# Performance work log

Measured on AMD Instinct MI355X. Metric: run time of the kernel, lower is better.

Reference implementation:

```python
import jax, jax.numpy as jnp
import numpy as np

B, DIM, H, W = 8, 128, 64, 64
K = 7                      # involution kernel size
PAD = (K - 1) // 2
GC = 16                    # group_channels (RedNet involution default)
G = DIM // GC              # groups = 8
RED = 4                    # reduction_ratio
BN_EPS = 1e-5
LN_EPS = 1e-6


def setup_inputs() -> dict:
    key = jax.random.key(0)
    ks = jax.random.split(key, 8)
    s = lambda k, sh: jax.random.normal(k, sh, jnp.float32) * 0.02
    return {
        "x": jax.random.normal(ks[0], (B, DIM, H, W), jnp.float32),
        # involution kernel-generation branch: 1x1 conv -> BN -> ReLU -> 1x1 conv
        "conv1_w": s(ks[1], (DIM // RED, DIM)), "conv1_b": jnp.zeros((DIM // RED,), jnp.float32),
        "bn_g": jnp.ones((DIM // RED,), jnp.float32), "bn_b": jnp.zeros((DIM // RED,), jnp.float32),
        "bn_mean": jnp.zeros((DIM // RED,), jnp.float32), "bn_var": jnp.ones((DIM // RED,), jnp.float32),
        "conv2_w": s(ks[2], (K * K * G, DIM // RED)), "conv2_b": jnp.zeros((K * K * G,), jnp.float32),
        # LayerNorm (channels_last)
        "ln_g": jnp.ones((DIM,), jnp.float32), "ln_b": jnp.zeros((DIM,), jnp.float32),
        # pointwise MLP
        "pw1_w": s(ks[3], (2 * DIM, DIM)), "pw1_b": jnp.zeros((2 * DIM,), jnp.float32),
        "pw2_w": s(ks[4], (DIM, 2 * DIM)), "pw2_b": jnp.zeros((DIM,), jnp.float32),
    }


def _involution(x, conv1_w, conv1_b, bn_g, bn_b, bn_mean, bn_var, conv2_w, conv2_b):
    # kernel-generation: 1x1 conv -> BN(eval) -> ReLU -> 1x1 conv
    t = jnp.einsum('oc,bchw->bohw', conv1_w, x) + conv1_b[None, :, None, None]
    scale = bn_g * jax.lax.rsqrt(bn_var + BN_EPS)
    t = t * scale[None, :, None, None] + (bn_b - bn_mean * scale)[None, :, None, None]
    t = jax.nn.relu(t)
    wgt = jnp.einsum('oc,bchw->bohw', conv2_w, t) + conv2_b[None, :, None, None]
    wgt = wgt.reshape(B, G, K * K, H, W)            # per-pixel kernels
    # apply per-pixel kernel: accumulate over window offsets (no unfold materialization)
    xp = jnp.pad(x, ((0, 0), (0, 0), (PAD, PAD), (PAD, PAD)))
    xg = xp.reshape(B, G, GC, H + 2 * PAD, W + 2 * PAD)
    out = jnp.zeros((B, G, GC, H, W), x.dtype)
    for i in range(K):
        for j in range(K):
            patch = xg[:, :, :, i:i + H, j:j + W]   # [B,G,GC,H,W]
            out = out + wgt[:, :, i * K + j][:, :, None] * patch
    return out.reshape(B, DIM, H, W)


def reference(x, conv1_w, conv1_b, bn_g, bn_b, bn_mean, bn_var, conv2_w, conv2_b,
              ln_g, ln_b, pw1_w, pw1_b, pw2_w, pw2_b):
    identity = x
    y = _involution(x, conv1_w, conv1_b, bn_g, bn_b, bn_mean, bn_var, conv2_w, conv2_b)
    y = y.transpose(0, 2, 3, 1)                     # NCHW -> NHWC
    mu = jnp.mean(y, axis=-1, keepdims=True)
    var = jnp.var(y, axis=-1, keepdims=True)
    y = (y - mu) * jax.lax.rsqrt(var + LN_EPS) * ln_g + ln_b
    y = jnp.einsum('bhwc,fc->bhwf', y, pw1_w) + pw1_b
    y = jax.nn.gelu(y, approximate=False)           # torch nn.GELU default (erf)
    # dropout: inference mode -> identity
    y = jnp.einsum('bhwf,cf->bhwc', y, pw2_w) + pw2_b
    y = y.transpose(0, 3, 1, 2)                     # NHWC -> NCHW
    return y + identity
```

## Files before the change

### kernel.cpp

```cpp
#include <hip/hip_runtime.h>
#include <hip/hip_bf16.h>
#include <math.h>

#define Bn   8
#define DIM  128
#define Hs   64
#define Ws   64
#define PADn 3
#define GC   16
#define Gn   8
#define CMID 32
#define NW   392
#define NWP  416

typedef __bf16 bf16x8 __attribute__((ext_vector_type(8)));
typedef float  f32x4  __attribute__((ext_vector_type(4)));
typedef _Float16 h2v  __attribute__((ext_vector_type(2)));
typedef __fp16   fp16x2 __attribute__((ext_vector_type(2)));

__device__ __forceinline__ f32x4 mfma16(bf16x8 a, bf16x8 b, f32x4 c) {
    return __builtin_amdgcn_mfma_f32_16x16x32_bf16(a, b, c, 0, 0, 0);
}

__device__ __forceinline__ __bf16 tobf(float v) {
    __hip_bfloat16 h = __float2bfloat16(v);
    return *reinterpret_cast<__bf16*>(&h);
}

__device__ __forceinline__ unsigned su16(float f) {
    __hip_bfloat16 h = __float2bfloat16(f);
    return (unsigned)*reinterpret_cast<unsigned short*>(&h);
}

__device__ __forceinline__ unsigned pk2u(float a, float b) {
    fp16x2 p = __builtin_amdgcn_cvt_pkrtz(a, b);
    return __builtin_bit_cast(unsigned, p);
}

__device__ __forceinline__ float gelu_t(float v) {
    float u = 0.7978845608f * v * fmaf(0.044715f, v * v, 1.0f);
    float t = __builtin_amdgcn_exp2f(fminf(u, 30.f) * 2.885390082f);
    return v * t * __builtin_amdgcn_rcpf(t + 1.0f);
}

__global__ __launch_bounds__(256) void k0_cvt(const float* __restrict__ w1,
        const float* __restrict__ w2,
        const float* __restrict__ pw1, const float* __restrict__ pw2,
        const float* __restrict__ x,
        __hip_bfloat16* __restrict__ w1b, __hip_bfloat16* __restrict__ w2b,
        __hip_bfloat16* __restrict__ mw1b, __hip_bfloat16* __restrict__ mw2b,
        unsigned* __restrict__ xpair) {
    int T = blockIdx.x * 256 + threadIdx.x;
    if (T < 32768) {
        int i = T;
        if (i < CMID * DIM) w1b[i] = __float2bfloat16(w1[i]);
        if (i < NWP * CMID)
            w2b[i] = (i < NW * CMID) ? __float2bfloat16(w2[i]) : __float2bfloat16(0.f);
        {
            int f = i >> 7, j = i & 127;
            int t4 = j >> 5, k = j & 31;
            int g = k >> 2, pi = (k >> 1) & 1, sel = k & 1;
            mw1b[i] = __float2bfloat16(pw1[f * 128 + g * 16 + t4 * 2 + pi + 8 * sel]);
        }
        mw2b[i] = __float2bfloat16(pw2[i]);
    }
    int c8 = T >> 10;
    int p4 = (T & 1023) * 4;
    int bb = c8 >> 6, gg = (c8 >> 3) & 7, cc = c8 & 7;
    size_t src = ((size_t)(bb * DIM + gg * GC + cc)) * 4096 + p4;
    float4 lo = *(const float4*)&x[src];
    float4 hi = *(const float4*)&x[src + 8 * 4096];
    uint4 o;
    o.x = pk2u(lo.x, hi.x);
    o.y = pk2u(lo.y, hi.y);
    o.z = pk2u(lo.z, hi.z);
    o.w = pk2u(lo.w, hi.w);
    *(uint4*)&xpair[(size_t)c8 * 4096 + p4] = o;
}

__global__ __launch_bounds__(64) void k_all(const float* __restrict__ x,
        const unsigned* __restrict__ xpair,
        const __hip_bfloat16* __restrict__ w1b, const float* __restrict__ b1v,
        const float* __restrict__ bng, const float* __restrict__ bnb,
        const float* __restrict__ bnm, const float* __restrict__ bnv,
        const __hip_bfloat16* __restrict__ w2b, const float* __restrict__ b2v,
        const float* __restrict__ lng, const float* __restrict__ lnb,
        const __hip_bfloat16* __restrict__ mw1b, const float* __restrict__ mb1,
        const __hip_bfloat16* __restrict__ mw2b, const float* __restrict__ mb2,
        float* __restrict__ out) {
    __shared__ __align__(16) char uni[15368];
    h2v* xp    = (h2v*)uni;
    h2v* wgt2  = (h2v*)(uni + 10752);
    __hip_bfloat16* tsh = (__hip_bfloat16*)(uni + 14280);
    __hip_bfloat16* ylds = (__hip_bfloat16*)uni;
    __hip_bfloat16* zsh  = (__hip_bfloat16*)(uni + 4352);

    int bid = blockIdx.x;
    int b = bid & 7;
    int rest = bid >> 3;
    int h = rest >> 2, wq = rest & 3;
    int w0 = wq * 16;
    int lane = threadIdx.x;
    int l15 = lane & 15, l4 = lane >> 4;
    int px = l15, t4 = l4;

    int goff[20];
    unsigned short ldso[20];
#pragma unroll
    for (int e = 0; e < 20; ++e) {
        int i = lane + e * 64;
        int ccp = i / 154;
        int rem = i - ccp * 154;
        int r = rem / 22, col = rem - r * 22;
        int hh = h + r - PADn, wc = w0 + col - PADn;
        bool ok = (i < 1232) & ((unsigned)hh < (unsigned)Hs) & ((unsigned)wc < (unsigned)Ws);
        goff[e] = ok ? (ccp * 4096 + hh * 64 + wc) : -1;
        ldso[e] = (unsigned short)(ccp * 168 + r * 24 + col);
    }

    auto stage = [&](int g, int buf) {
        const unsigned* xg = xpair + (size_t)(b * 64 + g * 8) * 4096;
        unsigned v[20];
#pragma unroll
        for (int e = 0; e < 20; ++e)
            v[e] = (goff[e] >= 0) ? xg[goff[e]] : 0u;
#pragma unroll
        for (int e = 0; e < 20; ++e)
            if (e < 19 || lane < 16)
                *(unsigned*)&xp[buf * 1344 + ldso[e]] = v[e];
    };

    bf16x8 afr[4];
#pragma unroll
    for (int ks = 0; ks < 4; ++ks)
#pragma unroll
        for (int i = 0; i < 8; ++i) {
            int c = ks * 32 + l4 * 8 + i;
            afr[ks][i] = tobf(x[(((size_t)b * DIM + c) * Hs + h) * Ws + w0 + l15]);
        }

    stage(0, 0);

    f32x4 acc1[2];
    acc1[0] = (f32x4){0.f, 0.f, 0.f, 0.f};
    acc1[1] = (f32x4){0.f, 0.f, 0.f, 0.f};
#pragma unroll
    for (int nt = 0; nt < 2; ++nt)
#pragma unroll
        for (int ks = 0; ks < 4; ++ks) {
            bf16x8 bf = *(const bf16x8*)&w1b[(nt * 16 + l15) * DIM + ks * 32 + l4 * 8];
            acc1[nt] = mfma16(afr[ks], bf, acc1[nt]);
        }
#pragma unroll
    for (int nt = 0; nt < 2; ++nt) {
        int o = nt * 16 + l15;
        float sc = bng[o] * rsqrtf(bnv[o] + 1e-5f);
        float sh = bnb[o] - bnm[o] * sc;
        float bv = b1v[o];
#pragma unroll
        for (int r = 0; r < 4; ++r) {
            float v = (acc1[nt][r] + bv) * sc + sh;
            tsh[(l4 * 4 + r) * 34 + o] = __float2bfloat16(fmaxf(v, 0.f));
        }
    }
    bf16x8 a_t = *(const bf16x8*)&tsh[l15 * 34 + l4 * 8];

    unsigned ypk[16];
    float s = 0.f, ss = 0.f;

#pragma unroll 1
    for (int g = 0; g < Gn; ++g) {
        int buf = g & 1;
        if (g == 0) ;
        else stage(g, buf);

        {
            f32x4 ac[4];
#pragma unroll
            for (int nt = 0; nt < 4; ++nt) ac[nt] = (f32x4){0.f, 0.f, 0.f, 0.f};
#pragma unroll
            for (int nt = 0; nt < 4; ++nt) {
                bf16x8 bf = *(const bf16x8*)&w2b[(size_t)(g * 49 + nt * 16 + l15) * CMID + l4 * 8];
                ac[nt] = mfma16(a_t, bf, ac[nt]);
            }
#pragma unroll
            for (int nt = 0; nt < 4; ++nt) {
                int p = nt * 16 + l15;
                if (p < 49) {
                    float bias = b2v[g * 49 + p];
#pragma unroll
                    for (int r = 0; r < 4; ++r) {
                        _Float16 hf16 = (_Float16)(ac[nt][r] + bias);
                        wgt2[p * 18 + l4 * 4 + r] = (h2v){hf16, hf16};
                    }
                }
            }
        }

        h2v wv[49];
#pragma unroll
        for (int p = 0; p < 49; ++p) wv[p] = wgt2[p * 18 + px];

#pragma unroll
        for (int pi = 0; pi < 2; ++pi) {
            int ccp = t4 * 2 + pi;
            const h2v* xrow = xp + buf * 1344 + ccp * 168;
            float accx = 0.f, accy = 0.f;
#pragma unroll
            for (int r = 0; r < 7; ++r) {
                h2v hacc = (h2v){(_Float16)0.f, (_Float16)0.f};
#pragma unroll
                for (int j = 0; j < 7; ++j)
                    hacc = wv[r * 7 + j] * xrow[r * 24 + px + j] + hacc;
                accx += (float)hacc.x;
                accy += (float)hacc.y;
            }
            ypk[g * 2 + pi] = su16(accx) | (su16(accy) << 16);
            s += accx + accy;
            ss = fmaf(accx, accx, fmaf(accy, accy, ss));
        }
    }

    s += __shfl_xor(s, 16);  s += __shfl_xor(s, 32);
    ss += __shfl_xor(ss, 16); ss += __shfl_xor(ss, 32);
    float mu = s * (1.f / DIM);
    float var = ss * (1.f / DIM) - mu * mu;
    float rs = rsqrtf(var + 1e-6f);

    {
        unsigned wds[16];
#pragma unroll
        for (int g = 0; g < 8; ++g)
#pragma unroll
            for (int pi = 0; pi < 2; ++pi) {
                unsigned wk = ypk[g * 2 + pi];
                float lo = __uint_as_float(wk << 16);
                float hi = __uint_as_float(wk & 0xffff0000u);
                int c0 = g * 16 + t4 * 2 + pi, c1 = c0 + 8;
                lo = (lo - mu) * rs * lng[c0] + lnb[c0];
                hi = (hi - mu) * rs * lng[c1] + lnb[c1];
                wds[g * 2 + pi] = su16(lo) | (su16(hi) << 16);
            }
        __hip_bfloat16* dst = ylds + px * 136 + t4 * 32;
#pragma unroll
        for (int c4 = 0; c4 < 4; ++c4) {
            uint4 vv;
            vv.x = wds[c4 * 4 + 0];
            vv.y = wds[c4 * 4 + 1];
            vv.z = wds[c4 * 4 + 2];
            vv.w = wds[c4 * 4 + 3];
            *(uint4*)&dst[(c4 ^ (px & 3)) << 3] = vv;
        }
    }

    bf16x8 ay[4];
#pragma unroll
    for (int ks = 0; ks < 4; ++ks)
        ay[ks] = *(const bf16x8*)&ylds[l15 * 136 + ks * 32 + ((l4 ^ (l15 & 3)) << 3)];

#pragma unroll
    for (int half = 0; half < 2; ++half) {
        f32x4 zac[8];
#pragma unroll
        for (int n = 0; n < 8; ++n) zac[n] = (f32x4){0.f, 0.f, 0.f, 0.f};
#pragma unroll
        for (int ks = 0; ks < 4; ++ks)
#pragma unroll
            for (int n = 0; n < 8; ++n) {
                int nt = half * 8 + n;
                bf16x8 bf = *(const bf16x8*)&mw1b[(nt * 16 + l15) * DIM + ks * 32 + l4 * 8];
                zac[n] = mfma16(ay[ks], bf, zac[n]);
            }
#pragma unroll
        for (int n = 0; n < 8; ++n) {
            int nt = half * 8 + n;
            float bv = mb1[nt * 16 + l15];
#pragma unroll
            for (int r = 0; r < 4; ++r) {
                float v = gelu_t(zac[n][r] + bv);
                zsh[(l4 * 4 + r) * 264 + nt * 16 + l15] = __float2bfloat16(v);
            }
        }
    }

    bf16x8 az[8];
#pragma unroll
    for (int ks = 0; ks < 8; ++ks)
        az[ks] = *(const bf16x8*)&zsh[l15 * 264 + ks * 32 + l4 * 8];

    f32x4 oac[8];
#pragma unroll
    for (int n = 0; n < 8; ++n) oac[n] = (f32x4){0.f, 0.f, 0.f, 0.f};
#pragma unroll
    for (int ks = 0; ks < 8; ++ks)
#pragma unroll
        for (int n = 0; n < 8; ++n) {
            bf16x8 bf = *(const bf16x8*)&mw2b[(n * 16 + l15) * 256 + ks * 32 + l4 * 8];
            oac[n] = mfma16(az[ks], bf, oac[n]);
        }

    float4 xr[8];
#pragma unroll
    for (int n = 0; n < 8; ++n) {
        int c = n * 16 + l15;
        xr[n] = *(const float4*)&x[(((size_t)b * DIM + c) * Hs + h) * Ws + w0 + l4 * 4];
    }
#pragma unroll
    for (int n = 0; n < 8; ++n) {
        int c = n * 16 + l15;
        float bv = mb2[c];
        size_t gi = (((size_t)b * DIM + c) * Hs + h) * Ws + w0 + l4 * 4;
        float4 o;
        o.x = oac[n][0] + bv + xr[n].x;
        o.y = oac[n][1] + bv + xr[n].y;
        o.z = oac[n][2] + bv + xr[n].z;
        o.w = oac[n][3] + bv + xr[n].w;
        *(float4*)&out[gi] = o;
    }
}

extern "C" void kernel_launch(void* const* d_in, const int* in_sizes, int n_in,
                              void* d_out, int out_size, void* d_ws, size_t ws_size,
                              hipStream_t stream) {
    const float* x       = (const float*)d_in[0];
    const float* conv1_w = (const float*)d_in[1];
    const float* conv1_b = (const float*)d_in[2];
    const float* bn_g    = (const float*)d_in[3];
    const float* bn_b    = (const float*)d_in[4];
    const float* bn_mean = (const float*)d_in[5];
    const float* bn_var  = (const float*)d_in[6];
    const float* conv2_w = (const float*)d_in[7];
    const float* conv2_b = (const float*)d_in[8];
    const float* ln_g    = (const float*)d_in[9];
    const float* ln_b    = (const float*)d_in[10];
    const float* pw1_w   = (const float*)d_in[11];
    const float* pw1_b   = (const float*)d_in[12];
    const float* pw2_w   = (const float*)d_in[13];
    const float* pw2_b   = (const float*)d_in[14];
    float* out = (float*)d_out;

    char* ws = (char*)d_ws;
    __hip_bfloat16* w1b  = (__hip_bfloat16*)ws;
    __hip_bfloat16* w2b  = (__hip_bfloat16*)(ws + 8192);
    __hip_bfloat16* mw1b = (__hip_bfloat16*)(ws + 34816);
    __hip_bfloat16* mw2b = (__hip_bfloat16*)(ws + 100352);
    unsigned* xpair      = (unsigned*)(ws + (1 << 20));

    hipLaunchKernelGGL(k0_cvt, dim3(2048), dim3(256), 0, stream,
                       conv1_w, conv2_w, pw1_w, pw2_w, x,
                       w1b, w2b, mw1b, mw2b, xpair);
    hipLaunchKernelGGL(k_all, dim3(Bn * Hs * 4), dim3(64), 0, stream,
                       x, xpair, w1b, conv1_b, bn_g, bn_b, bn_mean, bn_var,
                       w2b, conv2_b, ln_g, ln_b,
                       mw1b, pw1_b, mw2b, pw2_b, out);
}
```

Baseline: 70.60 us.

## Split fused block across two waves and stage from pre-padded input

The fused kernel now runs two 64-lane waves per block instead of one. Each wave handles four of the eight involution groups, half of the first MLP's output tiles and half of the second MLP's output tiles, with LayerNorm partial sums combined through shared memory and __syncthreads. The preprocessing kernel now writes a zero-padded 70x72 fp16-pair copy of x. This lets the staging loads skip bounds checks and use 8-byte loads, and the per-wave prefetch of the next group is now held in registers. The intent is to raise per-block parallelism and cut the serial per-block latency, at the cost of extra block barriers, more shared memory and a larger padded workspace.

```diff
diff --git a/kernel.cpp b/kernel.cpp
--- a/kernel.cpp
+++ b/kernel.cpp
@@ -6,7 +6,6 @@
 #define DIM  128
 #define Hs   64
 #define Ws   64
-#define PADn 3
 #define GC   16
 #define Gn   8
 #define CMID 32
@@ -21,22 +20,18 @@
 __device__ __forceinline__ f32x4 mfma16(bf16x8 a, bf16x8 b, f32x4 c) {
     return __builtin_amdgcn_mfma_f32_16x16x32_bf16(a, b, c, 0, 0, 0);
 }
-
 __device__ __forceinline__ __bf16 tobf(float v) {
     __hip_bfloat16 h = __float2bfloat16(v);
     return *reinterpret_cast<__bf16*>(&h);
 }
-
 __device__ __forceinline__ unsigned su16(float f) {
     __hip_bfloat16 h = __float2bfloat16(f);
     return (unsigned)*reinterpret_cast<unsigned short*>(&h);
 }
-
 __device__ __forceinline__ unsigned pk2u(float a, float b) {
     fp16x2 p = __builtin_amdgcn_cvt_pkrtz(a, b);
     return __builtin_bit_cast(unsigned, p);
 }
-
 __device__ __forceinline__ float gelu_t(float v) {
     float u = 0.7978845608f * v * fmaf(0.044715f, v * v, 1.0f);
     float t = __builtin_amdgcn_exp2f(fminf(u, 30.f) * 2.885390082f);
@@ -49,7 +44,7 @@
         const float* __restrict__ x,
         __hip_bfloat16* __restrict__ w1b, __hip_bfloat16* __restrict__ w2b,
         __hip_bfloat16* __restrict__ mw1b, __hip_bfloat16* __restrict__ mw2b,
-        unsigned* __restrict__ xpair) {
+        unsigned* __restrict__ xpad) {
     int T = blockIdx.x * 256 + threadIdx.x;
     if (T < 32768) {
         int i = T;
@@ -58,28 +53,33 @@
             w2b[i] = (i < NW * CMID) ? __float2bfloat16(w2[i]) : __float2bfloat16(0.f);
         {
             int f = i >> 7, j = i & 127;
-            int t4 = j >> 5, k = j & 31;
-            int g = k >> 2, pi = (k >> 1) & 1, sel = k & 1;
-            mw1b[i] = __float2bfloat16(pw1[f * 128 + g * 16 + t4 * 2 + pi + 8 * sel]);
+            int wv = j >> 6, t4 = (j >> 4) & 3, gl = (j >> 2) & 3;
+            int pi = (j >> 1) & 1, sel = j & 1;
+            mw1b[i] = __float2bfloat16(pw1[f * 128 + (wv * 4 + gl) * 16 + t4 * 2 + pi + 8 * sel]);
         }
         mw2b[i] = __float2bfloat16(pw2[i]);
     }
-    int c8 = T >> 10;
-    int p4 = (T & 1023) * 4;
-    int bb = c8 >> 6, gg = (c8 >> 3) & 7, cc = c8 & 7;
-    size_t src = ((size_t)(bb * DIM + gg * GC + cc)) * 4096 + p4;
-    float4 lo = *(const float4*)&x[src];
-    float4 hi = *(const float4*)&x[src + 8 * 4096];
-    uint4 o;
-    o.x = pk2u(lo.x, hi.x);
-    o.y = pk2u(lo.y, hi.y);
-    o.z = pk2u(lo.z, hi.z);
-    o.w = pk2u(lo.w, hi.w);
-    *(uint4*)&xpair[(size_t)c8 * 4096 + p4] = o;
-}
-
-__global__ __launch_bounds__(64) void k_all(const float* __restrict__ x,
-        const unsigned* __restrict__ xpair,
+#pragma unroll
+    for (int e = 0; e < 5; ++e) {
+        int idx = T + e * 524288;
+        if (idx < 512 * 5040) {
+            int c8 = idx / 5040;
+            int rem = idx - c8 * 5040;
+            int prow = rem / 72, pcol = rem - prow * 72;
+            int hh = prow - 3, wc = pcol - 3;
+            int bb = c8 >> 6, gg = (c8 >> 3) & 7, cc = c8 & 7;
+            unsigned v = 0;
+            if ((unsigned)hh < 64u && (unsigned)wc < 64u) {
+                size_t src = ((size_t)(bb * DIM + gg * GC + cc)) * 4096 + hh * 64 + wc;
+                v = pk2u(x[src], x[src + 8 * 4096]);
+            }
+            xpad[(size_t)c8 * 5040 + rem] = v;
+        }
+    }
+}
+
+__global__ __launch_bounds__(128) void k_all(const float* __restrict__ x,
+        const unsigned* __restrict__ xpad,
         const __hip_bfloat16* __restrict__ w1b, const float* __restrict__ b1v,
         const float* __restrict__ bng, const float* __restrict__ bnb,
         const float* __restrict__ bnm, const float* __restrict__ bnv,
@@ -88,10 +88,11 @@
         const __hip_bfloat16* __restrict__ mw1b, const float* __restrict__ mb1,
         const __hip_bfloat16* __restrict__ mw2b, const float* __restrict__ mb2,
         float* __restrict__ out) {
-    __shared__ __align__(16) char uni[15368];
-    h2v* xp    = (h2v*)uni;
-    h2v* wgt2  = (h2v*)(uni + 10752);
-    __hip_bfloat16* tsh = (__hip_bfloat16*)(uni + 14280);
+    __shared__ __align__(16) char uni[18944];
+    __shared__ float psA[32], psB[32];
+    __hip_bfloat16* tsh = (__hip_bfloat16*)uni;
+    h2v* xp   = (h2v*)(uni + 1088);
+    h2v* wgt2 = (h2v*)(uni + 11840);
     __hip_bfloat16* ylds = (__hip_bfloat16*)uni;
     __hip_bfloat16* zsh  = (__hip_bfloat16*)(uni + 4352);
 
@@ -100,34 +101,40 @@
     int rest = bid >> 3;
     int h = rest >> 2, wq = rest & 3;
     int w0 = wq * 16;
-    int lane = threadIdx.x;
+    int tid = threadIdx.x, lane = tid & 63, w = tid >> 6;
     int l15 = lane & 15, l4 = lane >> 4;
     int px = l15, t4 = l4;
 
-    int goff[20];
-    unsigned short ldso[20];
-#pragma unroll
-    for (int e = 0; e < 20; ++e) {
+    h2v* xpw = xp + w * 1344;
+    h2v* wgw = wgt2 + w * 882;
+
+    int goff[10];
+    unsigned short ldso[10];
+#pragma unroll
+    for (int e = 0; e < 10; ++e) {
         int i = lane + e * 64;
-        int ccp = i / 154;
-        int rem = i - ccp * 154;
-        int r = rem / 22, col = rem - r * 22;
-        int hh = h + r - PADn, wc = w0 + col - PADn;
-        bool ok = (i < 1232) & ((unsigned)hh < (unsigned)Hs) & ((unsigned)wc < (unsigned)Ws);
-        goff[e] = ok ? (ccp * 4096 + hh * 64 + wc) : -1;
-        ldso[e] = (unsigned short)(ccp * 168 + r * 24 + col);
-    }
-
-    auto stage = [&](int g, int buf) {
-        const unsigned* xg = xpair + (size_t)(b * 64 + g * 8) * 4096;
-        unsigned v[20];
-#pragma unroll
-        for (int e = 0; e < 20; ++e)
-            v[e] = (goff[e] >= 0) ? xg[goff[e]] : 0u;
-#pragma unroll
-        for (int e = 0; e < 20; ++e)
-            if (e < 19 || lane < 16)
-                *(unsigned*)&xp[buf * 1344 + ldso[e]] = v[e];
+        bool ok = i < 616;
+        int ii = ok ? i : 0;
+        int ccp = ii / 77;
+        int rem = ii - ccp * 77;
+        int r = rem / 11, pr = rem - r * 11;
+        goff[e] = ccp * 5040 + (h + r) * 72 + w0 + pr * 2;
+        ldso[e] = (unsigned short)(ccp * 168 + r * 24 + pr * 2);
+    }
+
+    auto stageLoad = [&](int g, uint2* v) {
+        const unsigned* xg = xpad + (size_t)(b * 64 + g * 8) * 5040;
+#pragma unroll
+        for (int e = 0; e < 10; ++e)
+            v[e] = *(const uint2*)&xg[goff[e]];
+    };
+    auto stageWrite = [&](uint2* v) {
+#pragma unroll
+        for (int e = 0; e < 10; ++e)
+            if (e < 9 || lane < 40) {
+                xpw[ldso[e]]     = __builtin_bit_cast(h2v, v[e].x);
+                xpw[ldso[e] + 1] = __builtin_bit_cast(h2v, v[e].y);
+            }
     };
 
     bf16x8 afr[4];
@@ -138,41 +145,37 @@
             int c = ks * 32 + l4 * 8 + i;
             afr[ks][i] = tobf(x[(((size_t)b * DIM + c) * Hs + h) * Ws + w0 + l15]);
         }
-
-    stage(0, 0);
-
-    f32x4 acc1[2];
-    acc1[0] = (f32x4){0.f, 0.f, 0.f, 0.f};
-    acc1[1] = (f32x4){0.f, 0.f, 0.f, 0.f};
-#pragma unroll
-    for (int nt = 0; nt < 2; ++nt)
+    {
+        uint2 v[10];
+        stageLoad(w * 4, v);
+        f32x4 acc1 = (f32x4){0.f, 0.f, 0.f, 0.f};
 #pragma unroll
         for (int ks = 0; ks < 4; ++ks) {
-            bf16x8 bf = *(const bf16x8*)&w1b[(nt * 16 + l15) * DIM + ks * 32 + l4 * 8];
-            acc1[nt] = mfma16(afr[ks], bf, acc1[nt]);
-        }
-#pragma unroll
-    for (int nt = 0; nt < 2; ++nt) {
-        int o = nt * 16 + l15;
+            bf16x8 bf = *(const bf16x8*)&w1b[(w * 16 + l15) * DIM + ks * 32 + l4 * 8];
+            acc1 = mfma16(afr[ks], bf, acc1);
+        }
+        int o = w * 16 + l15;
         float sc = bng[o] * rsqrtf(bnv[o] + 1e-5f);
         float sh = bnb[o] - bnm[o] * sc;
         float bv = b1v[o];
 #pragma unroll
         for (int r = 0; r < 4; ++r) {
-            float v = (acc1[nt][r] + bv) * sc + sh;
-            tsh[(l4 * 4 + r) * 34 + o] = __float2bfloat16(fmaxf(v, 0.f));
-        }
-    }
+            float vv = (acc1[r] + bv) * sc + sh;
+            tsh[(l4 * 4 + r) * 34 + o] = __float2bfloat16(fmaxf(vv, 0.f));
+        }
+        stageWrite(v);
+    }
+    __syncthreads();
     bf16x8 a_t = *(const bf16x8*)&tsh[l15 * 34 + l4 * 8];
 
-    unsigned ypk[16];
+    unsigned ypk[8];
     float s = 0.f, ss = 0.f;
 
 #pragma unroll 1
-    for (int g = 0; g < Gn; ++g) {
-        int buf = g & 1;
-        if (g == 0) ;
-        else stage(g, buf);
+    for (int gl = 0; gl < 4; ++gl) {
+        int g = w * 4 + gl;
+        uint2 vN[10];
+        if (gl < 3) stageLoad(g + 1, vN);
 
         {
             f32x4 ac[4];
@@ -191,75 +194,99 @@
 #pragma unroll
                     for (int r = 0; r < 4; ++r) {
                         _Float16 hf16 = (_Float16)(ac[nt][r] + bias);
-                        wgt2[p * 18 + l4 * 4 + r] = (h2v){hf16, hf16};
+                        wgw[p * 18 + l4 * 4 + r] = (h2v){hf16, hf16};
                     }
                 }
             }
         }
 
-        h2v wv[49];
-#pragma unroll
-        for (int p = 0; p < 49; ++p) wv[p] = wgt2[p * 18 + px];
-
-#pragma unroll
-        for (int pi = 0; pi < 2; ++pi) {
-            int ccp = t4 * 2 + pi;
-            const h2v* xrow = xp + buf * 1344 + ccp * 168;
-            float accx = 0.f, accy = 0.f;
-#pragma unroll
-            for (int r = 0; r < 7; ++r) {
-                h2v hacc = (h2v){(_Float16)0.f, (_Float16)0.f};
-#pragma unroll
-                for (int j = 0; j < 7; ++j)
-                    hacc = wv[r * 7 + j] * xrow[r * 24 + px + j] + hacc;
-                accx += (float)hacc.x;
-                accy += (float)hacc.y;
-            }
-            ypk[g * 2 + pi] = su16(accx) | (su16(accy) << 16);
-            s += accx + accy;
-            ss = fmaf(accx, accx, fmaf(accy, accy, ss));
-        }
+        float a00 = 0.f, a01 = 0.f, a10 = 0.f, a11 = 0.f;
+        {
+            h2v wv[28];
+#pragma unroll
+            for (int p = 0; p < 28; ++p) wv[p] = wgw[p * 18 + px];
+#pragma unroll
+            for (int pi = 0; pi < 2; ++pi) {
+                const h2v* xrow = xpw + (t4 * 2 + pi) * 168;
+                float ax = 0.f, ay2 = 0.f;
+#pragma unroll
+                for (int r = 0; r < 4; ++r) {
+                    h2v hacc = (h2v){(_Float16)0.f, (_Float16)0.f};
+#pragma unroll
+                    for (int j = 0; j < 7; ++j)
+                        hacc = wv[r * 7 + j] * xrow[r * 24 + px + j] + hacc;
+                    ax += (float)hacc.x;
+                    ay2 += (float)hacc.y;
+                }
+                if (pi == 0) { a00 = ax; a01 = ay2; } else { a10 = ax; a11 = ay2; }
+            }
+        }
+        {
+            h2v wv[21];
+#pragma unroll
+            for (int p = 0; p < 21; ++p) wv[p] = wgw[(28 + p) * 18 + px];
+#pragma unroll
+            for (int pi = 0; pi < 2; ++pi) {
+                const h2v* xrow = xpw + (t4 * 2 + pi) * 168;
+                float ax = 0.f, ay2 = 0.f;
+#pragma unroll
+                for (int r = 0; r < 3; ++r) {
+                    h2v hacc = (h2v){(_Float16)0.f, (_Float16)0.f};
+#pragma unroll
+                    for (int j = 0; j < 7; ++j)
+                        hacc = wv[r * 7 + j] * xrow[(r + 4) * 24 + px + j] + hacc;
+                    ax += (float)hacc.x;
+                    ay2 += (float)hacc.y;
+                }
+                if (pi == 0) { a00 += ax; a01 += ay2; } else { a10 += ax; a11 += ay2; }
+            }
+        }
+        ypk[gl * 2]     = su16(a00) | (su16(a01) << 16);
+        ypk[gl * 2 + 1] = su16(a10) | (su16(a11) << 16);
+        s += (a00 + a01) + (a10 + a11);
+        ss = fmaf(a00, a00, fmaf(a01, a01, fmaf(a10, a10, fmaf(a11, a11, ss))));
+
+        if (gl < 3) stageWrite(vN);
     }
 
     s += __shfl_xor(s, 16);  s += __shfl_xor(s, 32);
     ss += __shfl_xor(ss, 16); ss += __shfl_xor(ss, 32);
-    float mu = s * (1.f / DIM);
-    float var = ss * (1.f / DIM) - mu * mu;
+    if (lane < 16) { psA[w * 16 + px] = s; psB[w * 16 + px] = ss; }
+    __syncthreads();
+    float sa = psA[px] + psA[16 + px];
+    float sb = psB[px] + psB[16 + px];
+    float mu = sa * (1.f / DIM);
+    float var = sb * (1.f / DIM) - mu * mu;
     float rs = rsqrtf(var + 1e-6f);
 
     {
-        unsigned wds[16];
-#pragma unroll
-        for (int g = 0; g < 8; ++g)
+        unsigned wds[8];
+#pragma unroll
+        for (int gl = 0; gl < 4; ++gl)
 #pragma unroll
             for (int pi = 0; pi < 2; ++pi) {
-                unsigned wk = ypk[g * 2 + pi];
+                unsigned wk = ypk[gl * 2 + pi];
                 float lo = __uint_as_float(wk << 16);
                 float hi = __uint_as_float(wk & 0xffff0000u);
-                int c0 = g * 16 + t4 * 2 + pi, c1 = c0 + 8;
+                int c0 = (w * 4 + gl) * 16 + t4 * 2 + pi, c1 = c0 + 8;
                 lo = (lo - mu) * rs * lng[c0] + lnb[c0];
                 hi = (hi - mu) * rs * lng[c1] + lnb[c1];
-                wds[g * 2 + pi] = su16(lo) | (su16(hi) << 16);
-            }
-        __hip_bfloat16* dst = ylds + px * 136 + t4 * 32;
-#pragma unroll
-        for (int c4 = 0; c4 < 4; ++c4) {
-            uint4 vv;
-            vv.x = wds[c4 * 4 + 0];
-            vv.y = wds[c4 * 4 + 1];
-            vv.z = wds[c4 * 4 + 2];
-            vv.w = wds[c4 * 4 + 3];
-            *(uint4*)&dst[(c4 ^ (px & 3)) << 3] = vv;
-        }
-    }
+                wds[gl * 2 + pi] = su16(lo) | (su16(hi) << 16);
+            }
+        __hip_bfloat16* dst = ylds + px * 136 + w * 64 + t4 * 16;
+        uint4 v1 = {wds[0], wds[1], wds[2], wds[3]};
+        uint4 v2 = {wds[4], wds[5], wds[6], wds[7]};
+        *(uint4*)&dst[0] = v1;
+        *(uint4*)&dst[8] = v2;
+    }
+    __syncthreads();
 
     bf16x8 ay[4];
 #pragma unroll
     for (int ks = 0; ks < 4; ++ks)
-        ay[ks] = *(const bf16x8*)&ylds[l15 * 136 + ks * 32 + ((l4 ^ (l15 & 3)) << 3)];
-
-#pragma unroll
-    for (int half = 0; half < 2; ++half) {
+        ay[ks] = *(const bf16x8*)&ylds[l15 * 136 + ks * 32 + l4 * 8];
+
+    {
         f32x4 zac[8];
 #pragma unroll
         for (int n = 0; n < 8; ++n) zac[n] = (f32x4){0.f, 0.f, 0.f, 0.f};
@@ -267,47 +294,49 @@
         for (int ks = 0; ks < 4; ++ks)
 #pragma unroll
             for (int n = 0; n < 8; ++n) {
-                int nt = half * 8 + n;
+                int nt = w * 8 + n;
                 bf16x8 bf = *(const bf16x8*)&mw1b[(nt * 16 + l15) * DIM + ks * 32 + l4 * 8];
                 zac[n] = mfma16(ay[ks], bf, zac[n]);
             }
 #pragma unroll
         for (int n = 0; n < 8; ++n) {
-            int nt = half * 8 + n;
+            int nt = w * 8 + n;
             float bv = mb1[nt * 16 + l15];
 #pragma unroll
             for (int r = 0; r < 4; ++r) {
-                float v = gelu_t(zac[n][r] + bv);
-                zsh[(l4 * 4 + r) * 264 + nt * 16 + l15] = __float2bfloat16(v);
-            }
-        }
-    }
+                float vv = gelu_t(zac[n][r] + bv);
+                zsh[(l4 * 4 + r) * 264 + nt * 16 + l15] = __float2bfloat16(vv);
+            }
+        }
+    }
+    __syncthreads();
 
     bf16x8 az[8];
 #pragma unroll
     for (int ks = 0; ks < 8; ++ks)
         az[ks] = *(const bf16x8*)&zsh[l15 * 264 + ks * 32 + l4 * 8];
 
-    f32x4 oac[8];
-#pragma unroll
-    for (int n = 0; n < 8; ++n) oac[n] = (f32x4){0.f, 0.f, 0.f, 0.f};
+    f32x4 oac[4];
+#pragma unroll
+    for (int n = 0; n < 4; ++n) oac[n] = (f32x4){0.f, 0.f, 0.f, 0.f};
 #pragma unroll
     for (int ks = 0; ks < 8; ++ks)
 #pragma unroll
-        for (int n = 0; n < 8; ++n) {
-            bf16x8 bf = *(const bf16x8*)&mw2b[(n * 16 + l15) * 256 + ks * 32 + l4 * 8];
+        for (int n = 0; n < 4; ++n) {
+            int nt = w * 4 + n;
+            bf16x8 bf = *(const bf16x8*)&mw2b[(nt * 16 + l15) * 256 + ks * 32 + l4 * 8];
             oac[n] = mfma16(az[ks], bf, oac[n]);
         }
 
-    float4 xr[8];
-#pragma unroll
-    for (int n = 0; n < 8; ++n) {
-        int c = n * 16 + l15;
+    float4 xr[4];
+#pragma unroll
+    for (int n = 0; n < 4; ++n) {
+        int c = (w * 4 + n) * 16 + l15;
         xr[n] = *(const float4*)&x[(((size_t)b * DIM + c) * Hs + h) * Ws + w0 + l4 * 4];
     }
 #pragma unroll
-    for (int n = 0; n < 8; ++n) {
-        int c = n * 16 + l15;
+    for (int n = 0; n < 4; ++n) {
+        int c = (w * 4 + n) * 16 + l15;
         float bv = mb2[c];
         size_t gi = (((size_t)b * DIM + c) * Hs + h) * Ws + w0 + l4 * 4;
         float4 o;
@@ -344,13 +373,13 @@
     __hip_bfloat16* w2b  = (__hip_bfloat16*)(ws + 8192);
     __hip_bfloat16* mw1b = (__hip_bfloat16*)(ws + 34816);
     __hip_bfloat16* mw2b = (__hip_bfloat16*)(ws + 100352);
-    unsigned* xpair      = (unsigned*)(ws + (1 << 20));
+    unsigned* xpad       = (unsigned*)(ws + (1 << 20));
 
     hipLaunchKernelGGL(k0_cvt, dim3(2048), dim3(256), 0, stream,
                        conv1_w, conv2_w, pw1_w, pw2_w, x,
-                       w1b, w2b, mw1b, mw2b, xpair);
-    hipLaunchKernelGGL(k_all, dim3(Bn * Hs * 4), dim3(64), 0, stream,
-                       x, xpair, w1b, conv1_b, bn_g, bn_b, bn_mean, bn_var,
+                       w1b, w2b, mw1b, mw2b, xpad);
+    hipLaunchKernelGGL(k_all, dim3(Bn * Hs * 4), dim3(128), 0, stream,
+                       x, xpad, w1b, conv1_b, bn_g, bn_b, bn_mean, bn_var,
                        w2b, conv2_b, ln_g, ln_b,
                        mw1b, pw1_b, mw2b, pw2_b, out);
 }
```

Measured after the change: 86.84 us. 23.0% more time.

## Pre-pad input in global memory and use DPP lane shifts instead of LDS window staging

Applied to the files above, without the earlier changes.

The prep kernel now writes a zero-padded 70x72 fp16-pair copy of x, so the main kernel can load each window row straight from global memory without bounds checks. Neighbouring taps come from DPP row-shift operations across lanes instead of an LDS staging buffer. The per-pixel weights are stored transposed in LDS and read as 16-byte vectors, and the XOR swizzle on the LayerNorm output buffer is removed. This trades LDS traffic for more global loads and register pressure, and the padded buffer adds write traffic in the prep kernel.

```diff
diff --git a/kernel.cpp b/kernel.cpp
--- a/kernel.cpp
+++ b/kernel.cpp
@@ -6,7 +6,6 @@
 #define DIM  128
 #define Hs   64
 #define Ws   64
-#define PADn 3
 #define GC   16
 #define Gn   8
 #define CMID 32
@@ -21,22 +20,19 @@
 __device__ __forceinline__ f32x4 mfma16(bf16x8 a, bf16x8 b, f32x4 c) {
     return __builtin_amdgcn_mfma_f32_16x16x32_bf16(a, b, c, 0, 0, 0);
 }
-
 __device__ __forceinline__ __bf16 tobf(float v) {
     __hip_bfloat16 h = __float2bfloat16(v);
     return *reinterpret_cast<__bf16*>(&h);
 }
-
 __device__ __forceinline__ unsigned su16(float f) {
     __hip_bfloat16 h = __float2bfloat16(f);
     return (unsigned)*reinterpret_cast<unsigned short*>(&h);
 }
-
 __device__ __forceinline__ unsigned pk2u(float a, float b) {
     fp16x2 p = __builtin_amdgcn_cvt_pkrtz(a, b);
     return __builtin_bit_cast(unsigned, p);
 }
-
+__device__ __forceinline__ h2v u2h(unsigned u) { return __builtin_bit_cast(h2v, u); }
 __device__ __forceinline__ float gelu_t(float v) {
     float u = 0.7978845608f * v * fmaf(0.044715f, v * v, 1.0f);
     float t = __builtin_amdgcn_exp2f(fminf(u, 30.f) * 2.885390082f);
@@ -49,7 +45,7 @@
         const float* __restrict__ x,
         __hip_bfloat16* __restrict__ w1b, __hip_bfloat16* __restrict__ w2b,
         __hip_bfloat16* __restrict__ mw1b, __hip_bfloat16* __restrict__ mw2b,
-        unsigned* __restrict__ xpair) {
+        unsigned* __restrict__ xpad) {
     int T = blockIdx.x * 256 + threadIdx.x;
     if (T < 32768) {
         int i = T;
@@ -64,22 +60,27 @@
         }
         mw2b[i] = __float2bfloat16(pw2[i]);
     }
-    int c8 = T >> 10;
-    int p4 = (T & 1023) * 4;
-    int bb = c8 >> 6, gg = (c8 >> 3) & 7, cc = c8 & 7;
-    size_t src = ((size_t)(bb * DIM + gg * GC + cc)) * 4096 + p4;
-    float4 lo = *(const float4*)&x[src];
-    float4 hi = *(const float4*)&x[src + 8 * 4096];
-    uint4 o;
-    o.x = pk2u(lo.x, hi.x);
-    o.y = pk2u(lo.y, hi.y);
-    o.z = pk2u(lo.z, hi.z);
-    o.w = pk2u(lo.w, hi.w);
-    *(uint4*)&xpair[(size_t)c8 * 4096 + p4] = o;
+#pragma unroll
+    for (int e = 0; e < 5; ++e) {
+        int idx = T + e * 524288;
+        if (idx < 512 * 5040) {
+            int c8 = idx / 5040;
+            int rem = idx - c8 * 5040;
+            int prow = rem / 72, pcol = rem - prow * 72;
+            int hh = prow - 3, wc = pcol - 3;
+            int bb = c8 >> 6, gg = (c8 >> 3) & 7, cc = c8 & 7;
+            unsigned v = 0;
+            if ((unsigned)hh < 64u && (unsigned)wc < 64u) {
+                size_t src = ((size_t)(bb * DIM + gg * GC + cc)) * 4096 + hh * 64 + wc;
+                v = pk2u(x[src], x[src + 8 * 4096]);
+            }
+            xpad[(size_t)c8 * 5040 + rem] = v;
+        }
+    }
 }
 
 __global__ __launch_bounds__(64) void k_all(const float* __restrict__ x,
-        const unsigned* __restrict__ xpair,
+        const unsigned* __restrict__ xpad,
         const __hip_bfloat16* __restrict__ w1b, const float* __restrict__ b1v,
         const float* __restrict__ bng, const float* __restrict__ bnb,
         const float* __restrict__ bnm, const float* __restrict__ bnv,
@@ -88,12 +89,11 @@
         const __hip_bfloat16* __restrict__ mw1b, const float* __restrict__ mb1,
         const __hip_bfloat16* __restrict__ mw2b, const float* __restrict__ mb2,
         float* __restrict__ out) {
-    __shared__ __align__(16) char uni[15368];
-    h2v* xp    = (h2v*)uni;
-    h2v* wgt2  = (h2v*)(uni + 10752);
-    __hip_bfloat16* tsh = (__hip_bfloat16*)(uni + 14280);
-    __hip_bfloat16* ylds = (__hip_bfloat16*)uni;
-    __hip_bfloat16* zsh  = (__hip_bfloat16*)(uni + 4352);
+    __shared__ __align__(16) char uni[17216];
+    __hip_bfloat16* tsh   = (__hip_bfloat16*)uni;
+    h2v*            wgt2T = (h2v*)(uni + 1088);
+    __hip_bfloat16* ylds  = (__hip_bfloat16*)(uni + 4416);
+    __hip_bfloat16* zsh   = (__hip_bfloat16*)(uni + 8768);
 
     int bid = blockIdx.x;
     int b = bid & 7;
@@ -104,32 +104,6 @@
     int l15 = lane & 15, l4 = lane >> 4;
     int px = l15, t4 = l4;
 
-    int goff[20];
-    unsigned short ldso[20];
-#pragma unroll
-    for (int e = 0; e < 20; ++e) {
-        int i = lane + e * 64;
-        int ccp = i / 154;
-        int rem = i - ccp * 154;
-        int r = rem / 22, col = rem - r * 22;
-        int hh = h + r - PADn, wc = w0 + col - PADn;
-        bool ok = (i < 1232) & ((unsigned)hh < (unsigned)Hs) & ((unsigned)wc < (unsigned)Ws);
-        goff[e] = ok ? (ccp * 4096 + hh * 64 + wc) : -1;
-        ldso[e] = (unsigned short)(ccp * 168 + r * 24 + col);
-    }
-
-    auto stage = [&](int g, int buf) {
-        const unsigned* xg = xpair + (size_t)(b * 64 + g * 8) * 4096;
-        unsigned v[20];
-#pragma unroll
-        for (int e = 0; e < 20; ++e)
-            v[e] = (goff[e] >= 0) ? xg[goff[e]] : 0u;
-#pragma unroll
-        for (int e = 0; e < 20; ++e)
-            if (e < 19 || lane < 16)
-                *(unsigned*)&xp[buf * 1344 + ldso[e]] = v[e];
-    };
-
     bf16x8 afr[4];
 #pragma unroll
     for (int ks = 0; ks < 4; ++ks)
@@ -138,9 +112,6 @@
             int c = ks * 32 + l4 * 8 + i;
             afr[ks][i] = tobf(x[(((size_t)b * DIM + c) * Hs + h) * Ws + w0 + l15]);
         }
-
-    stage(0, 0);
-
     f32x4 acc1[2];
     acc1[0] = (f32x4){0.f, 0.f, 0.f, 0.f};
     acc1[1] = (f32x4){0.f, 0.f, 0.f, 0.f};
@@ -170,9 +141,16 @@
 
 #pragma unroll 1
     for (int g = 0; g < Gn; ++g) {
-        int buf = g & 1;
-        if (g == 0) ;
-        else stage(g, buf);
+        unsigned Ax[14], Bx[14];
+#pragma unroll
+        for (int pi = 0; pi < 2; ++pi)
+#pragma unroll
+            for (int r = 0; r < 7; ++r) {
+                const unsigned* rp = xpad + (size_t)(b * 64 + g * 8 + t4 * 2 + pi) * 5040
+                                   + (h + r) * 72 + w0;
+                Ax[pi * 7 + r] = rp[px];
+                Bx[pi * 7 + r] = rp[px + 16];
+            }
 
         {
             f32x4 ac[4];
@@ -191,33 +169,51 @@
 #pragma unroll
                     for (int r = 0; r < 4; ++r) {
                         _Float16 hf16 = (_Float16)(ac[nt][r] + bias);
-                        wgt2[p * 18 + l4 * 4 + r] = (h2v){hf16, hf16};
+                        wgt2T[(l4 * 4 + r) * 52 + p] = (h2v){hf16, hf16};
                     }
                 }
             }
         }
 
-        h2v wv[49];
-#pragma unroll
-        for (int p = 0; p < 49; ++p) wv[p] = wgt2[p * 18 + px];
-
+        h2v wv[52];
+#pragma unroll
+        for (int u = 0; u < 13; ++u) {
+            uint4 t = *(const uint4*)&wgt2T[px * 52 + u * 4];
+            wv[u * 4 + 0] = u2h(t.x);
+            wv[u * 4 + 1] = u2h(t.y);
+            wv[u * 4 + 2] = u2h(t.z);
+            wv[u * 4 + 3] = u2h(t.w);
+        }
+
+#define INV_TAP(J)                                                                          \
+        {                                                                                   \
+            unsigned ta = (unsigned)__builtin_amdgcn_update_dpp(                            \
+                0, (int)A, 0x100 + J, 0xF, 0xF, false);                                     \
+            unsigned tb = (unsigned)__builtin_amdgcn_update_dpp(                            \
+                0, (int)B, 0x110 + (16 - J), 0xF, 0xF, false);                              \
+            hacc = wv[r * 7 + J] * u2h(ta | tb) + hacc;                                     \
+        }
+        float acc[2][2];
 #pragma unroll
         for (int pi = 0; pi < 2; ++pi) {
-            int ccp = t4 * 2 + pi;
-            const h2v* xrow = xp + buf * 1344 + ccp * 168;
-            float accx = 0.f, accy = 0.f;
+            float ax = 0.f, ay2 = 0.f;
 #pragma unroll
             for (int r = 0; r < 7; ++r) {
-                h2v hacc = (h2v){(_Float16)0.f, (_Float16)0.f};
-#pragma unroll
-                for (int j = 0; j < 7; ++j)
-                    hacc = wv[r * 7 + j] * xrow[r * 24 + px + j] + hacc;
-                accx += (float)hacc.x;
-                accy += (float)hacc.y;
-            }
-            ypk[g * 2 + pi] = su16(accx) | (su16(accy) << 16);
-            s += accx + accy;
-            ss = fmaf(accx, accx, fmaf(accy, accy, ss));
+                unsigned A = Ax[pi * 7 + r], B = Bx[pi * 7 + r];
+                h2v hacc = wv[r * 7] * u2h(A);
+                INV_TAP(1) INV_TAP(2) INV_TAP(3)
+                INV_TAP(4) INV_TAP(5) INV_TAP(6)
+                ax += (float)hacc.x;
+                ay2 += (float)hacc.y;
+            }
+            acc[pi][0] = ax; acc[pi][1] = ay2;
+        }
+#undef INV_TAP
+#pragma unroll
+        for (int pi = 0; pi < 2; ++pi) {
+            ypk[g * 2 + pi] = su16(acc[pi][0]) | (su16(acc[pi][1]) << 16);
+            s += acc[pi][0] + acc[pi][1];
+            ss = fmaf(acc[pi][0], acc[pi][0], fmaf(acc[pi][1], acc[pi][1], ss));
         }
     }
 
@@ -244,19 +240,15 @@
         __hip_bfloat16* dst = ylds + px * 136 + t4 * 32;
 #pragma unroll
         for (int c4 = 0; c4 < 4; ++c4) {
-            uint4 vv;
-            vv.x = wds[c4 * 4 + 0];
-            vv.y = wds[c4 * 4 + 1];
-            vv.z = wds[c4 * 4 + 2];
-            vv.w = wds[c4 * 4 + 3];
-            *(uint4*)&dst[(c4 ^ (px & 3)) << 3] = vv;
+            uint4 vv = {wds[c4 * 4 + 0], wds[c4 * 4 + 1], wds[c4 * 4 + 2], wds[c4 * 4 + 3]};
+            *(uint4*)&dst[c4 * 8] = vv;
         }
     }
 
     bf16x8 ay[4];
 #pragma unroll
     for (int ks = 0; ks < 4; ++ks)
-        ay[ks] = *(const bf16x8*)&ylds[l15 * 136 + ks * 32 + ((l4 ^ (l15 & 3)) << 3)];
+        ay[ks] = *(const bf16x8*)&ylds[l15 * 136 + ks * 32 + l4 * 8];
 
 #pragma unroll
     for (int half = 0; half < 2; ++half) {
@@ -344,13 +336,13 @@
     __hip_bfloat16* w2b  = (__hip_bfloat16*)(ws + 8192);
     __hip_bfloat16* mw1b = (__hip_bfloat16*)(ws + 34816);
     __hip_bfloat16* mw2b = (__hip_bfloat16*)(ws + 100352);
-    unsigned* xpair      = (unsigned*)(ws + (1 << 20));
+    unsigned* xpad       = (unsigned*)(ws + (1 << 20));
 
     hipLaunchKernelGGL(k0_cvt, dim3(2048), dim3(256), 0, stream,
                        conv1_w, conv2_w, pw1_w, pw2_w, x,
-                       w1b, w2b, mw1b, mw2b, xpair);
+                       w1b, w2b, mw1b, mw2b, xpad);
     hipLaunchKernelGGL(k_all, dim3(Bn * Hs * 4), dim3(64), 0, stream,
-                       x, xpair, w1b, conv1_b, bn_g, bn_b, bn_mean, bn_var,
+                       x, xpad, w1b, conv1_b, bn_g, bn_b, bn_mean, bn_var,
                        w2b, conv2_b, ln_g, ln_b,
                        mw1b, pw1_b, mw2b, pw2_b, out);
 }
```

New measurement: 67.17 us. -4.9%, faster.
